# Optimization experiments

Measured on AMD Instinct MI355X. Metric: run time of the kernel, lower is better.

The kernel has to match this reference:

```python
import jax, jax.numpy as jnp
import numpy as np

B, S, D = 8, 512, 1024
E, F, K = 8, 4096, 2


def setup_inputs() -> dict:
    key = jax.random.key(0)
    ks = jax.random.split(key, 8)
    scale = 1.0 / np.sqrt(D)
    return {
        "x": jax.random.normal(ks[0], (B, S, D), jnp.float32),
        "y": jax.random.randint(ks[1], (B,), 0, D),
        "W": jax.random.normal(ks[2], (D, D), jnp.float32) * scale,
        "b": jnp.zeros((D,), jnp.float32),
        "Wg": jax.random.normal(ks[3], (D, E), jnp.float32) * scale,
        "w1": jax.random.normal(ks[4], (E, D, F), jnp.float32) * scale,
        "b1": jnp.zeros((E, F), jnp.float32),
        "w2": jax.random.normal(ks[5], (E, F, D), jnp.float32) * (1.0 / np.sqrt(F)),
        "b2": jnp.zeros((E, D), jnp.float32),
    }


def reference(x, y, W, b, Wg, w1, b1, w2, b2):
    # linear projection (torch Linear convention: x @ W.T + b)
    lin = jnp.einsum("bsd,ed->bse", x, W) + b                      # [B,S,D]

    # --- MoE: top-2 softmax gate, renormalized over the top-k ---
    gate_logits = jnp.einsum("bsd,de->bse", lin, Wg)               # [B,S,E]
    probs = jax.nn.softmax(gate_logits, axis=-1)
    top_p, top_i = jax.lax.top_k(probs, K)                          # [B,S,K]
    top_p = top_p / jnp.sum(top_p, axis=-1, keepdims=True)
    # combine weights per expert: scatter top-k probs back to [B,S,E]
    gate = jnp.sum(jax.nn.one_hot(top_i, E, dtype=lin.dtype) * top_p[..., None], axis=-2)  # [B,S,E]

    # expert FFNs evaluated densely, combined by (sparse) gate weights
    h = jax.nn.relu(jnp.einsum("bsd,edf->ebsf", lin, w1) + b1[:, None, None, :])  # [E,B,S,F]
    expert_out = jnp.einsum("ebsf,efd->ebsd", h, w2) + b2[:, None, None, :]        # [E,B,S,D]
    moe_out = jnp.einsum("bse,ebsd->bsd", gate, expert_out)                        # [B,S,D]

    # residual, mean pool over sequence, cross-entropy
    sent_emb = jnp.mean(x + moe_out, axis=1)                       # [B,D] used as logits
    logp = jax.nn.log_softmax(sent_emb, axis=-1)
    loss = -jnp.mean(logp[jnp.arange(B), y])
    return loss
```

## Files before the change

### kernel.cpp

```cpp
#include <hip/hip_runtime.h>

#define TOK 4096
#define DD  1024
#define NE  8
#define FF  4096
#define NB  8
#define SS  512
#define HROWS 8320

typedef unsigned short ushort_t;
typedef __attribute__((ext_vector_type(8))) short bshort8;
typedef __attribute__((ext_vector_type(4))) float floatx4;

__device__ __forceinline__ ushort_t f2bf(float f) {
  unsigned int u = __float_as_uint(f);
  u += 0x7fffu + ((u >> 16) & 1u);
  return (ushort_t)(u >> 16);
}
__device__ __forceinline__ float bf2f(ushort_t h) {
  return __uint_as_float(((unsigned int)h) << 16);
}

__device__ __forceinline__ void gl_lds16(const ushort_t* g, ushort_t* l) {
  __builtin_amdgcn_global_load_lds(
      (const __attribute__((address_space(1))) unsigned int*)g,
      (__attribute__((address_space(3))) unsigned int*)l, 16, 0, 0);
}

__global__ __launch_bounds__(256) void k_cast(
    const float* __restrict__ in, ushort_t* __restrict__ out, int n4) {
  int i = blockIdx.x * 256 + threadIdx.x;
  if (i < n4) {
    float4 v = ((const float4*)in)[i];
    ushort4 o;
    o.x = f2bf(v.x); o.y = f2bf(v.y); o.z = f2bf(v.z); o.w = f2bf(v.w);
    ((ushort4*)out)[i] = o;
  }
}

__global__ __launch_bounds__(256) void k_transpose_cast(
    const float* __restrict__ in, size_t in_estride, int in_rstride,
    ushort_t* __restrict__ out, size_t out_estride, int out_rstride) {
  __shared__ ushort_t t[64][70];
  const float* ib = in + blockIdx.z * in_estride;
  ushort_t* ob = out + blockIdx.z * out_estride;
  const int r0 = blockIdx.y * 64, c0 = blockIdx.x * 64;
  const int tid = threadIdx.x;
  const int lr = tid >> 4, lc4 = (tid & 15) * 4;
#pragma unroll
  for (int it = 0; it < 4; ++it) {
    int r = lr + it * 16;
    float4 v = *(const float4*)&ib[(size_t)(r0 + r) * in_rstride + c0 + lc4];
    t[r][lc4 + 0] = f2bf(v.x);
    t[r][lc4 + 1] = f2bf(v.y);
    t[r][lc4 + 2] = f2bf(v.z);
    t[r][lc4 + 3] = f2bf(v.w);
  }
  __syncthreads();
  const int oc = tid >> 5, od2 = (tid & 31) * 2;
#pragma unroll
  for (int it = 0; it < 8; ++it) {
    int cc = oc + it * 8;
    ushort2 w;
    w.x = t[od2 + 0][cc];
    w.y = t[od2 + 1][cc];
    *(ushort2*)&ob[(size_t)(c0 + cc) * out_rstride + r0 + od2] = w;
  }
}

template <int MODE>
__global__ __launch_bounds__(256) void k_mfma(
    const ushort_t* __restrict__ A, const ushort_t* __restrict__ Bm,
    const float* __restrict__ bias, ushort_t* __restrict__ Obf,
    float* __restrict__ Of, const int* __restrict__ cnt,
    const int* __restrict__ offs, const int* __restrict__ btok, int f0,
    int accum, int kext, int ast, int ost, size_t bstride) {
  const int e = (MODE == 0) ? 0 : blockIdx.z;
  int c = TOK, off = 0;
  if (MODE != 0) {
    c = cnt[e];
    off = offs[e];
    if ((int)blockIdx.y * 128 >= c) return;
  }
  const int m0 = blockIdx.y * 128;
  const int n0 = blockIdx.x * 128;
  const ushort_t* Bp = (MODE == 0) ? Bm : Bm + (size_t)e * bstride;

  __shared__ ushort_t Als[2][128 * 32];
  __shared__ ushort_t Bls[2][128 * 32];
  __shared__ int ts[128];

  const int tid = threadIdx.x;
  if (tid < 128) {
    int p = m0 + tid;
    int r;
    if (MODE == 0) r = p;
    else if (MODE == 1) r = btok[e * TOK + min(p, c - 1)];
    else r = off + p;
    ts[tid] = r;
  }
  __syncthreads();

  const int lane = tid & 63;
  const int w = tid >> 6;
  const int wm = (w & 1) * 64, wn = (w >> 1) * 64;
  const int lm = lane & 15, lq = lane >> 4;
  const int sr = lane >> 2;
  const int sg = lane & 3;

  const int r0 = w * 32 + sr;
  const int r1 = r0 + 16;
  const int q = (sg - (r0 >> 1)) & 3;
  const int d0 = r0 * 32 + sg * 8;
  const int d1 = r1 * 32 + sg * 8;
  const ushort_t* sA0 = A + (size_t)ts[r0] * ast + q * 8;
  const ushort_t* sA1 = A + (size_t)ts[r1] * ast + q * 8;
  const ushort_t* sB0 = Bp + (size_t)(n0 + r0) * kext + q * 8;
  const ushort_t* sB1 = Bp + (size_t)(n0 + r1) * kext + q * 8;

#define STG(bi, kk)                       \
  do {                                    \
    gl_lds16(sA0 + (kk), &Als[bi][d0]);   \
    gl_lds16(sA1 + (kk), &Als[bi][d1]);   \
    gl_lds16(sB0 + (kk), &Bls[bi][d0]);   \
    gl_lds16(sB1 + (kk), &Bls[bi][d1]);   \
  } while (0)

  floatx4 zero = {0.f, 0.f, 0.f, 0.f};
  floatx4 acc[4][4];
#pragma unroll
  for (int i = 0; i < 4; ++i)
#pragma unroll
    for (int j = 0; j < 4; ++j) acc[i][j] = zero;

  STG(0, 0);
  __syncthreads();

  int cur = 0;
  for (int k0 = 0; k0 < kext; k0 += 32) {
    if (k0 + 32 < kext) STG(cur ^ 1, k0 + 32);

    const ushort_t* Ab = Als[cur];
    const ushort_t* Bb = Bls[cur];
    bshort8 af[4], bfr[4];
#pragma unroll
    for (int i = 0; i < 4; ++i) {
      int r = wm + i * 16 + lm;
      af[i] = *(const bshort8*)&Ab[r * 32 + (((lq + (r >> 1)) & 3) * 8)];
    }
#pragma unroll
    for (int j = 0; j < 4; ++j) {
      int r = wn + j * 16 + lm;
      bfr[j] = *(const bshort8*)&Bb[r * 32 + (((lq + (r >> 1)) & 3) * 8)];
    }
#pragma unroll
    for (int i = 0; i < 4; ++i)
#pragma unroll
      for (int j = 0; j < 4; ++j)
        acc[i][j] = __builtin_amdgcn_mfma_f32_16x16x32_bf16(af[i], bfr[j],
                                                            acc[i][j], 0, 0, 0);

    __syncthreads();
    cur ^= 1;
  }
#undef STG

#pragma unroll
  for (int i = 0; i < 4; ++i) {
#pragma unroll
    for (int j = 0; j < 4; ++j) {
      int n = wn + j * 16 + lm;
#pragma unroll
      for (int rr = 0; rr < 4; ++rr) {
        int m = wm + i * 16 + lq * 4 + rr;
        float v = acc[i][j][rr];
        if (MODE == 0) {
          int gn = n0 + n;
          v += bias[gn];
          Obf[(size_t)(m0 + m) * DD + gn] = f2bf(v);
        } else if (MODE == 1) {
          int p = m0 + m;
          if (p < c) {
            int gn = n0 + n;
            v += bias[(size_t)e * FF + f0 + gn];
            v = fmaxf(v, 0.f);
            Obf[(size_t)(off + p) * ost + gn] = f2bf(v);
          }
        } else {
          int p = m0 + m;
          if (p < c) {
            int gn = n0 + n;
            if (!accum) v += bias[(size_t)e * DD + gn];
            float* dp = &Of[(size_t)(off + p) * DD + gn];
            if (accum) *dp += v; else *dp = v;
          }
        }
      }
    }
  }
}

__global__ __launch_bounds__(256) void k_logits(
    const ushort_t* __restrict__ lin_bf, const float* __restrict__ Wg,
    int* __restrict__ topi, float* __restrict__ wts) {
  const int wv = threadIdx.x >> 6, lane = threadIdx.x & 63;
  const int t = blockIdx.x * 4 + wv;
  float acc[NE] = {};
  const ushort_t* lr = lin_bf + (size_t)t * DD;
#pragma unroll 4
  for (int d0 = 0; d0 < DD; d0 += 64) {
    float v = bf2f(lr[d0 + lane]);
    const float* wgr = Wg + (size_t)(d0 + lane) * NE;
    float4 g0 = *(const float4*)(wgr);
    float4 g1 = *(const float4*)(wgr + 4);
    acc[0] += v * g0.x; acc[1] += v * g0.y; acc[2] += v * g0.z; acc[3] += v * g0.w;
    acc[4] += v * g1.x; acc[5] += v * g1.y; acc[6] += v * g1.z; acc[7] += v * g1.w;
  }
#pragma unroll
  for (int off = 32; off > 0; off >>= 1) {
#pragma unroll
    for (int e = 0; e < NE; ++e) acc[e] += __shfl_xor(acc[e], off);
  }
  if (lane == 0) {
    int i1 = 0;
#pragma unroll
    for (int e = 1; e < NE; ++e)
      if (acc[e] > acc[i1]) i1 = e;
    int i2 = (i1 == 0) ? 1 : 0;
#pragma unroll
    for (int e = 0; e < NE; ++e)
      if (e != i1 && acc[e] > acc[i2]) i2 = e;
    float r = __expf(acc[i2] - acc[i1]);
    topi[t] = i1 | (i2 << 4);
    wts[2 * t + 0] = 1.0f / (1.0f + r);
    wts[2 * t + 1] = r / (1.0f + r);
  }
}

#define RT 512
__global__ __launch_bounds__(RT) void k_route(
    const int* __restrict__ topi, int* __restrict__ cnt, int* __restrict__ offs,
    int* __restrict__ btok, int* __restrict__ eslot) {
  __shared__ int sc[NE][RT + 1];
  __shared__ int tot[NE];
  const int tid = threadIdx.x;
  int lc[NE] = {};
  int my[8];
#pragma unroll
  for (int i = 0; i < 8; ++i) {
    int t = tid * 8 + i;
    int p = topi[t];
    my[i] = p;
    lc[p & 15]++;
    lc[(p >> 4) & 15]++;
  }
#pragma unroll
  for (int e = 0; e < NE; ++e) sc[e][tid] = lc[e];
  __syncthreads();
  if (tid < NE) {
    int s = 0;
    for (int i = 0; i < RT; ++i) { int v = sc[tid][i]; sc[tid][i] = s; s += v; }
    tot[tid] = s;
  }
  __syncthreads();
  if (tid == 0) {
    int s = 0;
    for (int e = 0; e < NE; ++e) { offs[e] = s; cnt[e] = tot[e]; s += tot[e]; }
  }
  __syncthreads();
  int run[NE];
#pragma unroll
  for (int e = 0; e < NE; ++e) run[e] = sc[e][tid];
#pragma unroll
  for (int i = 0; i < 8; ++i) {
    int t = tid * 8 + i, p = my[i];
    int e1 = p & 15, e2 = (p >> 4) & 15;
    int s1 = run[e1]++;
    btok[e1 * TOK + s1] = t;
    eslot[2 * t + 0] = e1 * TOK + s1;
    int s2 = run[e2]++;
    btok[e2 * TOK + s2] = t;
    eslot[2 * t + 1] = e2 * TOK + s2;
  }
}

__global__ __launch_bounds__(256) void k_pool(
    const float* __restrict__ x, const float* __restrict__ ob,
    const int* __restrict__ offs, const int* __restrict__ eslot,
    const float* __restrict__ wts, float* __restrict__ sent) {
  const int b = blockIdx.y;
  const int d = blockIdx.x * 256 + threadIdx.x;
  const int sc = blockIdx.z;
  float a = 0.f;
  for (int s = sc * 64; s < sc * 64 + 64; ++s) {
    int t = b * SS + s;
    int e0 = eslot[2 * t], e1 = eslot[2 * t + 1];
    int g0 = offs[e0 >> 12] + (e0 & (TOK - 1));
    int g1 = offs[e1 >> 12] + (e1 & (TOK - 1));
    a += x[(size_t)t * DD + d] + wts[2 * t] * ob[(size_t)g0 * DD + d] +
         wts[2 * t + 1] * ob[(size_t)g1 * DD + d];
  }
  atomicAdd(&sent[b * DD + d], a * (1.0f / SS));
}

__global__ __launch_bounds__(1024) void k_loss(
    const float* __restrict__ sent, const int* __restrict__ y,
    float* __restrict__ out) {
  __shared__ float red[16];
  const int tid = threadIdx.x;
  const int lane = tid & 63, wv = tid >> 6;
  float loss = 0.f;
  for (int b = 0; b < NB; ++b) {
    float v = sent[b * DD + tid];
    float m = v;
#pragma unroll
    for (int off = 32; off > 0; off >>= 1) m = fmaxf(m, __shfl_xor(m, off));
    if (lane == 0) red[wv] = m;
    __syncthreads();
    float m2 = red[0];
#pragma unroll
    for (int w = 1; w < 16; ++w) m2 = fmaxf(m2, red[w]);
    __syncthreads();
    float ex = __expf(v - m2);
#pragma unroll
    for (int off = 32; off > 0; off >>= 1) ex += __shfl_xor(ex, off);
    if (lane == 0) red[wv] = ex;
    __syncthreads();
    if (tid == 0) {
      float se = 0.f;
      for (int w = 0; w < 16; ++w) se += red[w];
      loss += m2 + logf(se) - sent[b * DD + y[b]];
    }
    __syncthreads();
  }
  if (tid == 0) out[0] = loss / NB;
}

extern "C" void kernel_launch(void* const* d_in, const int* in_sizes, int n_in,
                              void* d_out, int out_size, void* d_ws,
                              size_t ws_size, hipStream_t stream) {
  const float* x  = (const float*)d_in[0];
  const int*   y  = (const int*)d_in[1];
  const float* W  = (const float*)d_in[2];
  const float* bb = (const float*)d_in[3];
  const float* Wg = (const float*)d_in[4];
  const float* w1 = (const float*)d_in[5];
  const float* b1 = (const float*)d_in[6];
  const float* w2 = (const float*)d_in[7];
  const float* b2 = (const float*)d_in[8];
  float* out = (float*)d_out;

  auto need = [](size_t FCr) -> size_t {
    size_t o = 0;
    auto al = [&](size_t b) { o = (o + b + 255) & ~255ull; };
    al((size_t)TOK * DD * 2);
    al((size_t)TOK * DD * 2);
    al((size_t)DD * DD * 2);
    al((size_t)HROWS * FCr * 2);
    al((size_t)NE * FCr * DD * 2);
    al((size_t)NE * DD * FCr * 2);
    al((size_t)HROWS * DD * 4);
    al((size_t)NE * TOK * 4);
    al(64); al(64);
    al((size_t)TOK * 4);
    al((size_t)2 * TOK * 4);
    al((size_t)2 * TOK * 4);
    al((size_t)NB * DD * 4);
    return o;
  };
  const int nchunks = (ws_size >= need(FF)) ? 1 : 4;
  const int FCr = FF / nchunks;

  char* base = (char*)d_ws;
  size_t o = 0;
  auto al = [&](size_t b) -> char* {
    char* p = base + o;
    o = (o + b + 255) & ~255ull;
    return p;
  };
  ushort_t* lin_bf = (ushort_t*)al((size_t)TOK * DD * 2);
  ushort_t* x_bf   = (ushort_t*)al((size_t)TOK * DD * 2);
  ushort_t* W_bf   = (ushort_t*)al((size_t)DD * DD * 2);
  ushort_t* h_bf   = (ushort_t*)al((size_t)HROWS * FCr * 2);
  ushort_t* w1t    = (ushort_t*)al((size_t)NE * FCr * DD * 2);
  ushort_t* w2t    = (ushort_t*)al((size_t)NE * DD * FCr * 2);
  float*    ob     = (float*)al((size_t)HROWS * DD * 4);
  int*      btok   = (int*)al((size_t)NE * TOK * 4);
  int*      cnt    = (int*)al(64);
  int*      offs   = (int*)al(64);
  int*      topi   = (int*)al((size_t)TOK * 4);
  int*      eslot  = (int*)al((size_t)2 * TOK * 4);
  float*    wts    = (float*)al((size_t)2 * TOK * 4);
  float*    sent   = (float*)al((size_t)NB * DD * 4);

  hipMemsetAsync(sent, 0, NB * DD * sizeof(float), stream);

  k_cast<<<TOK * DD / 4 / 256, 256, 0, stream>>>(x, x_bf, TOK * DD / 4);
  k_cast<<<DD * DD / 4 / 256, 256, 0, stream>>>(W, W_bf, DD * DD / 4);

  k_mfma<0><<<dim3(DD / 128, TOK / 128), 256, 0, stream>>>(
      x_bf, W_bf, bb, lin_bf, nullptr, nullptr, nullptr, nullptr, 0, 0,
      DD, DD, DD, 0);

  k_logits<<<TOK / 4, 256, 0, stream>>>(lin_bf, Wg, topi, wts);
  k_route<<<1, RT, 0, stream>>>(topi, cnt, offs, btok, eslot);

  for (int ci = 0; ci < nchunks; ++ci) {
    int f0 = ci * FCr;
    k_transpose_cast<<<dim3(FCr / 64, DD / 64, NE), 256, 0, stream>>>(
        w1 + f0, (size_t)DD * FF, FF, w1t, (size_t)FCr * DD, DD);
    k_mfma<1><<<dim3(FCr / 128, TOK / 128, NE), 256, 0, stream>>>(
        lin_bf, w1t, b1, h_bf, nullptr, cnt, offs, btok, f0, 0,
        DD, DD, FCr, (size_t)FCr * DD);
    k_transpose_cast<<<dim3(DD / 64, FCr / 64, NE), 256, 0, stream>>>(
        w2 + (size_t)f0 * DD, (size_t)FF * DD, DD, w2t, (size_t)DD * FCr, FCr);
    k_mfma<2><<<dim3(DD / 128, TOK / 128, NE), 256, 0, stream>>>(
        h_bf, w2t, b2, nullptr, ob, cnt, offs, btok, f0, ci > 0 ? 1 : 0,
        FCr, FCr, DD, (size_t)DD * FCr);
  }

  k_pool<<<dim3(DD / 256, NB, 8), 256, 0, stream>>>(x, ob, offs, eslot, wts,
                                                    sent);
  k_loss<<<1, 1024, 0, stream>>>(sent, y, out);
}
```

Baseline: 647.6 us.

## Triple-buffer LDS staging with manual waitcnt and remap workgroups across XCDs

Changes the GEMM main loop from double to triple LDS buffering. It prefetches two K-tiles ahead, replaces __syncthreads with explicit vmcnt waits and s_barrier, and issues the prefetch after the LDS fragment reads. It also remaps the flat workgroup index so consecutive tiles land on the same XCD, aiming for better L2 locality. The goal is to hide global-load latency and cut barrier stalls, at the cost of 50% more LDS, which may reduce occupancy. The hand-counted waitcnt values are a correctness risk.

```diff
diff --git a/kernel.cpp b/kernel.cpp
--- a/kernel.cpp
+++ b/kernel.cpp
@@ -75,19 +75,28 @@
     float* __restrict__ Of, const int* __restrict__ cnt,
     const int* __restrict__ offs, const int* __restrict__ btok, int f0,
     int accum, int kext, int ast, int ost, size_t bstride) {
-  const int e = (MODE == 0) ? 0 : blockIdx.z;
+  const int gx = gridDim.x, gy = gridDim.y;
+  int flat = blockIdx.x + gx * (blockIdx.y + gy * blockIdx.z);
+  const int nwg = gx * gy * (int)gridDim.z;
+  flat = (flat & 7) * (nwg >> 3) + (flat >> 3);
+  const int bx = flat % gx;
+  const int t2 = flat / gx;
+  const int by = t2 % gy;
+  const int bz = t2 / gy;
+
+  const int e = (MODE == 0) ? 0 : bz;
   int c = TOK, off = 0;
   if (MODE != 0) {
     c = cnt[e];
     off = offs[e];
-    if ((int)blockIdx.y * 128 >= c) return;
-  }
-  const int m0 = blockIdx.y * 128;
-  const int n0 = blockIdx.x * 128;
+    if (by * 128 >= c) return;
+  }
+  const int m0 = by * 128;
+  const int n0 = bx * 128;
   const ushort_t* Bp = (MODE == 0) ? Bm : Bm + (size_t)e * bstride;
 
-  __shared__ ushort_t Als[2][128 * 32];
-  __shared__ ushort_t Bls[2][128 * 32];
+  __shared__ ushort_t Als[3][128 * 32];
+  __shared__ ushort_t Bls[3][128 * 32];
   __shared__ int ts[128];
 
   const int tid = threadIdx.x;
@@ -118,12 +127,13 @@
   const ushort_t* sB0 = Bp + (size_t)(n0 + r0) * kext + q * 8;
   const ushort_t* sB1 = Bp + (size_t)(n0 + r1) * kext + q * 8;
 
-#define STG(bi, kk)                       \
-  do {                                    \
-    gl_lds16(sA0 + (kk), &Als[bi][d0]);   \
-    gl_lds16(sA1 + (kk), &Als[bi][d1]);   \
-    gl_lds16(sB0 + (kk), &Bls[bi][d0]);   \
-    gl_lds16(sB1 + (kk), &Bls[bi][d1]);   \
+#define STG(bi, kt)                            \
+  do {                                         \
+    const int ko_ = (kt) << 5;                 \
+    gl_lds16(sA0 + ko_, &Als[bi][d0]);         \
+    gl_lds16(sA1 + ko_, &Als[bi][d1]);         \
+    gl_lds16(sB0 + ko_, &Bls[bi][d0]);         \
+    gl_lds16(sB1 + ko_, &Bls[bi][d1]);         \
   } while (0)
 
   floatx4 zero = {0.f, 0.f, 0.f, 0.f};
@@ -133,13 +143,15 @@
 #pragma unroll
     for (int j = 0; j < 4; ++j) acc[i][j] = zero;
 
+  const int nk = kext >> 5;
+
   STG(0, 0);
-  __syncthreads();
+  STG(1, 1);
+  asm volatile("s_waitcnt vmcnt(4)" ::: "memory");
+  asm volatile("s_barrier" ::: "memory");
 
   int cur = 0;
-  for (int k0 = 0; k0 < kext; k0 += 32) {
-    if (k0 + 32 < kext) STG(cur ^ 1, k0 + 32);
-
+  for (int k = 0; k < nk; ++k) {
     const ushort_t* Ab = Als[cur];
     const ushort_t* Bb = Bls[cur];
     bshort8 af[4], bfr[4];
@@ -153,6 +165,12 @@
       int r = wn + j * 16 + lm;
       bfr[j] = *(const bshort8*)&Bb[r * 32 + (((lq + (r >> 1)) & 3) * 8)];
     }
+    int pf = cur + 2; if (pf >= 3) pf -= 3;
+    if (k + 2 < nk) STG(pf, k + 2);
+
+    asm volatile("s_waitcnt lgkmcnt(0)" ::: "memory");
+    __builtin_amdgcn_sched_barrier(0);
+
 #pragma unroll
     for (int i = 0; i < 4; ++i)
 #pragma unroll
@@ -160,8 +178,15 @@
         acc[i][j] = __builtin_amdgcn_mfma_f32_16x16x32_bf16(af[i], bfr[j],
                                                             acc[i][j], 0, 0, 0);
 
-    __syncthreads();
-    cur ^= 1;
+    if (k + 1 < nk) {
+      if (k + 2 < nk) {
+        asm volatile("s_waitcnt vmcnt(4)" ::: "memory");
+      } else {
+        asm volatile("s_waitcnt vmcnt(0)" ::: "memory");
+      }
+      asm volatile("s_barrier" ::: "memory");
+    }
+    cur += 1; if (cur >= 3) cur -= 3;
   }
 #undef STG
 
```

Measured after the change: 613.3 us. 1.06x faster.
